# Optimization experiments

Measured on AMD Instinct MI355X. Metric: run time of the kernel, lower is better.

## Reference

```python
import jax, jax.numpy as jnp
import numpy as np

B, L, P, TPP, D, G = 4, 2, 100, 64, 768, 10  # batch, layers, passages, tokens/passage, hidden, n_tables
T = P * TPP


def setup_inputs() -> dict:
    key = jax.random.key(0)
    ks = jax.random.split(key, 12)
    s = 0.02  # weight init scale
    return {
        "answer_states": jax.random.normal(ks[0], (B, L, 1, D), jnp.float32),
        "query_passage_states": jax.random.normal(ks[1], (B, L, T, D), jnp.float32),
        "passage_masks": (jax.random.uniform(ks[2], (B, P, TPP)) < 0.9).astype(jnp.float32),
        "table_ids": jax.random.randint(ks[3], (B, P), 0, G, dtype=jnp.int32),
        "fusion_scores": jax.random.normal(ks[4], (B, P), jnp.float32),
        # learned params: passage_fnt (3D->D), table_fnt (3D->D), feat_l1 (2D->D), feat_l2 (D->1)
        "W_p": jax.random.normal(ks[5], (3 * D, D), jnp.float32) * s,
        "b_p": jnp.zeros((D,), jnp.float32),
        "W_t": jax.random.normal(ks[6], (3 * D, D), jnp.float32) * s,
        "b_t": jnp.zeros((D,), jnp.float32),
        "W1": jax.random.normal(ks[7], (2 * D, D), jnp.float32) * s,
        "b1": jnp.zeros((D,), jnp.float32),
        "W2": jax.random.normal(ks[8], (D, 1), jnp.float32) * s,
        "b2": jnp.zeros((1,), jnp.float32),
    }


def reference(answer_states, query_passage_states, passage_masks, table_ids,
              fusion_scores, W_p, b_p, W_t, b_t, W1, b1, W2, b2):
    # Use only the last layer, as in forward (states[:, -1:, :, :]).
    a = answer_states[:, -1:, :, :]                 # [B,1,1,D]
    q = query_passage_states[:, -1:, :, :]          # [B,1,T,D]
    a = jnp.broadcast_to(a, q.shape)
    x = jnp.concatenate([a, q, a * q], axis=-1)     # [B,1,T,3D]

    ps = (x @ W_p + b_p).reshape(B, 1, P, TPP, D)   # passage states
    ts = (x @ W_t + b_t).reshape(B, 1, P, TPP, D)   # per-passage table states

    # Group-by table_id max-pool over the passage axis, then broadcast back.
    def aggr_one(ts_i, tid):                        # ts_i: [1,P,TPP,D], tid: [P]
        data = jnp.moveaxis(ts_i, 1, 0)             # [P,1,TPP,D]
        seg_max = jax.ops.segment_max(data, tid, num_segments=G)  # [G,1,TPP,D]
        return jnp.moveaxis(seg_max[tid], 0, 1)     # [1,P,TPP,D]

    aggr = jax.vmap(aggr_one)(ts, table_ids)        # [B,1,P,TPP,D]

    feat = jnp.concatenate([ps, aggr], axis=-1)     # [B,1,P,TPP,2D]
    # feature_fnt: Linear -> ReLU -> (dropout = identity in eval) -> Linear
    h = jax.nn.relu(feat @ W1 + b1)                 # [B,1,P,TPP,D]
    scores = (h @ W2 + b2)[..., 0]                  # [B,1,P,TPP]

    masked = scores * passage_masks[:, None, :, :]  # broadcast mask over layers
    # sum over layers and tokens -> per-passage adapt scores
    out = masked.sum(axis=(1, 3))                   # [B,P]
    return out
```

## Files before the change

kernel.cpp:

```cpp
#include <hip/hip_runtime.h>
#include <hip/hip_bf16.h>

#define B_ 4
#define L_ 2
#define P_ 100
#define TPP_ 64
#define D_ 768
#define G_ 10
#define T_ (P_ * TPP_)
#define NC_ (2 * D_)

typedef __attribute__((ext_vector_type(8))) short bf16x8;
typedef __attribute__((ext_vector_type(4))) float f32x4;

__device__ __forceinline__ unsigned short f2bf(float f) {
    __hip_bfloat16 h = __float2bfloat16(f);
    return *reinterpret_cast<unsigned short*>(&h);
}
__device__ __forceinline__ float bfu2f(unsigned short u) {
    return __uint_as_float(((unsigned int)u) << 16);
}

__device__ __forceinline__ void gload_lds16(const void* g, void* l) {
    __builtin_amdgcn_global_load_lds(
        (const __attribute__((address_space(1))) void*)g,
        (__attribute__((address_space(3))) void*)l, 16, 0, 0);
}

#define SBAR()   __builtin_amdgcn_s_barrier()
#define SCHEDB() __builtin_amdgcn_sched_barrier(0)
#define VMCNT4() asm volatile("s_waitcnt vmcnt(4)" ::: "memory")
#define VMCNT0() asm volatile("s_waitcnt vmcnt(0)" ::: "memory")

__device__ __forceinline__ unsigned int fenc(float v) {
    unsigned int bits = __float_as_uint(v);
    return bits ^ (unsigned int)(((int)bits >> 31) | 0x80000000);
}
__device__ __forceinline__ float fdec(unsigned int k) {
    unsigned int bits = (k & 0x80000000u) ? (k ^ 0x80000000u) : ~k;
    return __uint_as_float(bits);
}

__device__ __forceinline__ void stage64(
    const __hip_bfloat16* __restrict__ Ag, const __hip_bfloat16* __restrict__ Bg,
    int k0, __hip_bfloat16 (*As)[64], __hip_bfloat16 (*Bs)[64],
    int w, int row_l, int soff)
{
#pragma unroll
    for (int j = 0; j < 2; ++j) {
        int r = w * 16 + j * 8 + row_l;
        gload_lds16(Ag + (size_t)r * D_ + k0 + soff, &As[w * 16 + j * 8][0]);
        gload_lds16(Bg + (size_t)r * D_ + k0 + soff, &Bs[w * 16 + j * 8][0]);
    }
}

__device__ __forceinline__ void mfma_step64(
    __hip_bfloat16 (*As)[64], __hip_bfloat16 (*Bs)[64],
    int rr, int h, int wm, int wn, f32x4 acc[4][2])
{
#pragma unroll
    for (int ks = 0; ks < 2; ++ks) {
        const int rsl = (((ks << 2) + h) ^ (rr & 7)) << 3;
        bf16x8 af[4], bfr[2];
#pragma unroll
        for (int mi = 0; mi < 4; ++mi)
            af[mi] = *reinterpret_cast<const bf16x8*>(
                &As[wm * 64 + mi * 16 + rr][rsl]);
#pragma unroll
        for (int ni = 0; ni < 2; ++ni)
            bfr[ni] = *reinterpret_cast<const bf16x8*>(
                &Bs[wn * 32 + ni * 16 + rr][rsl]);
#pragma unroll
        for (int mi = 0; mi < 4; ++mi)
#pragma unroll
            for (int ni = 0; ni < 2; ++ni)
                acc[mi][ni] = __builtin_amdgcn_mfma_f32_16x16x32_bf16(
                    af[mi], bfr[ni], acc[mi][ni], 0, 0, 0);
    }
}

#define MFMA_STEP_P(As, Bs)                                                   \
    __builtin_amdgcn_s_setprio(1);                                            \
    mfma_step64(As, Bs, rr, h, wm, wn, acc);                                  \
    __builtin_amdgcn_s_setprio(0);

#define MFMA_LOOP_PIPE(Ag, Bg)                                                \
    {                                                                         \
        const int rr = lane & 15, h = lane >> 4;                              \
        const int row_l = lane >> 3;                                          \
        const int soff = ((lane & 7) ^ row_l) << 3;                           \
        stage64((Ag), (Bg), 0, As0, Bs0, w, row_l, soff);                     \
        stage64((Ag), (Bg), 64, As1, Bs1, w, row_l, soff);                    \
        SCHEDB();                                                             \
        for (int t = 0; t < 10; t += 2) {                                     \
            VMCNT4(); SBAR(); SCHEDB();                                       \
            MFMA_STEP_P(As0, Bs0);                                            \
            SCHEDB(); SBAR(); SCHEDB();                                       \
            stage64((Ag), (Bg), (t + 2) * 64, As0, Bs0, w, row_l, soff);      \
            SCHEDB();                                                         \
            VMCNT4(); SBAR(); SCHEDB();                                       \
            MFMA_STEP_P(As1, Bs1);                                            \
            SCHEDB(); SBAR(); SCHEDB();                                       \
            stage64((Ag), (Bg), (t + 3) * 64, As1, Bs1, w, row_l, soff);      \
            SCHEDB();                                                         \
        }                                                                     \
        VMCNT4(); SBAR(); SCHEDB();                                           \
        MFMA_STEP_P(As0, Bs0);                                   \
        SCHEDB();                                                             \
        VMCNT0(); SBAR(); SCHEDB();                                           \
        MFMA_STEP_P(As1, Bs1);                                   \
        __syncthreads();                                                      \
    }

#define DECL_LDS_DB()                                                         \
    __shared__ __align__(16) __hip_bfloat16 As0[128][64];                     \
    __shared__ __align__(16) __hip_bfloat16 Bs0[128][64];                     \
    __shared__ __align__(16) __hip_bfloat16 As1[128][64];                     \
    __shared__ __align__(16) __hip_bfloat16 Bs1[128][64];

#define DECL_ACC()                                                            \
    f32x4 acc[4][2];                                                          \
    _Pragma("unroll") for (int i = 0; i < 4; ++i)                             \
        _Pragma("unroll") for (int j = 0; j < 2; ++j)                         \
            _Pragma("unroll") for (int e = 0; e < 4; ++e) acc[i][j][e] = 0.0f;

__global__ __launch_bounds__(256) void prep_all(
    const float* __restrict__ answer, const float* __restrict__ W_p,
    const float* __restrict__ b_p, const float* __restrict__ W_t,
    const float* __restrict__ b_t, const float* __restrict__ W1,
    const float* __restrict__ qps, const float* __restrict__ mask,
    const float* __restrict__ b2,
    __hip_bfloat16* __restrict__ Wpe_nat, __hip_bfloat16* __restrict__ Wbig,
    float* __restrict__ c_p, float* __restrict__ c_t,
    __hip_bfloat16* __restrict__ qb, __hip_bfloat16* __restrict__ W1at,
    __hip_bfloat16* __restrict__ W1bt, unsigned int* __restrict__ smU,
    float* __restrict__ out)
{
    __shared__ float lds[64][65];
    __shared__ float a_s[64];
    __shared__ float red2[2][4][64];

    const int bid = blockIdx.x;
    const int tid = threadIdx.x;

    if (bid < 1152) {
        const int n0 = (bid % 24) * 64;
        const int k0 = ((bid / 24) % 12) * 64;
        const int b  = bid / 288;
        if (tid < 64) a_s[tid] = answer[((size_t)b * L_ + (L_ - 1)) * D_ + k0 + tid];
        __syncthreads();
        if (n0 < D_) {
#pragma unroll
            for (int i = 0; i < 16; ++i) {
                int k = (tid >> 6) + i * 4;
                int n = tid & 63;
                float v = W_p[(size_t)(D_ + k0 + k) * D_ + n0 + n] +
                          a_s[k] * W_p[(size_t)(2 * D_ + k0 + k) * D_ + n0 + n];
                Wpe_nat[(size_t)b * D_ * D_ + (size_t)(k0 + k) * D_ + n0 + n] =
                    __float2bfloat16(v);
            }
        } else {
            const int nn0 = n0 - D_;
#pragma unroll
            for (int i = 0; i < 16; ++i) {
                int k = (tid >> 6) + i * 4;
                int n = tid & 63;
                lds[k][n] = W_t[(size_t)(D_ + k0 + k) * D_ + nn0 + n] +
                            a_s[k] * W_t[(size_t)(2 * D_ + k0 + k) * D_ + nn0 + n];
            }
            __syncthreads();
#pragma unroll
            for (int j = 0; j < 16; ++j) {
                int n = (tid >> 6) + j * 4;
                int kk = tid & 63;
                Wbig[((size_t)b * NC_ + n0 + n) * D_ + k0 + kk] =
                    __float2bfloat16(lds[kk][n]);
            }
        }
    } else if (bid < 1200) {
        const int local = bid - 1152;
        const int b = local / 12;
        const int d = (local % 12) * 64 + (tid & 63);
        const int ks = tid >> 6;
        const float* a = answer + ((size_t)b * L_ + (L_ - 1)) * D_;
        float sp = 0.f, st = 0.f;
#pragma unroll 4
        for (int k = ks; k < D_; k += 4) {
            float av = a[k];
            sp += av * W_p[(size_t)k * D_ + d];
            st += av * W_t[(size_t)k * D_ + d];
        }
        red2[0][ks][tid & 63] = sp;
        red2[1][ks][tid & 63] = st;
        __syncthreads();
        if (ks == 0) {
            float s1 = b_p[d], s2 = b_t[d];
#pragma unroll
            for (int i = 0; i < 4; ++i) {
                s1 += red2[0][i][tid & 63];
                s2 += red2[1][i][tid & 63];
            }
            c_p[b * D_ + d] = s1;
            c_t[b * D_ + d] = s2;
        }
    } else if (bid < 1488) {
        const int local = bid - 1200;
        const int n0 = (local % 12) * 64;
        const int k0 = (local / 12) * 64;
#pragma unroll
        for (int i = 0; i < 16; ++i) {
            int k = (tid >> 6) + i * 4;
            int n = tid & 63;
            lds[k][n] = W1[(size_t)(k0 + k) * D_ + n0 + n];
        }
        __syncthreads();
        __hip_bfloat16* dst = (k0 < D_) ? W1at : W1bt;
        const int kk0 = (k0 < D_) ? k0 : k0 - D_;
#pragma unroll
        for (int j = 0; j < 16; ++j) {
            int n = (tid >> 6) + j * 4;
            int kk = tid & 63;
            dst[(size_t)(n0 + n) * D_ + kk0 + kk] = __float2bfloat16(lds[kk][n]);
        }
    } else if (bid < 1490) {
        int bp = (bid - 1488) * 256 + tid;
        if (bp < B_ * P_) {
            float s = 0.f;
#pragma unroll 8
            for (int t = 0; t < TPP_; ++t) s += mask[(size_t)bp * TPP_ + t];
            out[bp] = s * b2[0];
        }
    } else if (bid < 11090) {
        size_t base = ((size_t)(bid - 1490) * 256 + tid) * 8;
        int b = (int)(base / ((size_t)T_ * D_));
        size_t off = base % ((size_t)T_ * D_);
        const float4* src = reinterpret_cast<const float4*>(
            qps + ((size_t)b * L_ + (L_ - 1)) * (size_t)T_ * D_ + off);
        float4 v0 = src[0], v1 = src[1];
        bf16x8 o;
        o[0] = (short)f2bf(v0.x); o[1] = (short)f2bf(v0.y);
        o[2] = (short)f2bf(v0.z); o[3] = (short)f2bf(v0.w);
        o[4] = (short)f2bf(v1.x); o[5] = (short)f2bf(v1.y);
        o[6] = (short)f2bf(v1.z); o[7] = (short)f2bf(v1.w);
        *reinterpret_cast<bf16x8*>(&qb[base]) = o;
    } else {
        size_t base = ((size_t)(bid - 11090) * 256 + tid) * 8;
        uint4 z = {0u, 0u, 0u, 0u};
        *reinterpret_cast<uint4*>(&smU[base]) = z;
        *reinterpret_cast<uint4*>(&smU[base + 4]) = z;
    }
}

__global__ __launch_bounds__(512) void fused_ts_c1(
    const __hip_bfloat16* __restrict__ qb, __hip_bfloat16* __restrict__ Wbig,
    const float* __restrict__ c_t, const int* __restrict__ tids,
    unsigned int* __restrict__ smU,
    const __hip_bfloat16* __restrict__ W1at,
    const __hip_bfloat16* __restrict__ Wpe_nat,
    const float* __restrict__ c_p, const float* __restrict__ W1,
    const float* __restrict__ b1, float* __restrict__ cc)
{
    DECL_LDS_DB();
    __shared__ float red[8][64];
    const int bid = blockIdx.x;
    const int tid = threadIdx.x;
    const int lane = tid & 63, w = tid >> 6;
    const int wm = w & 1, wn = w >> 1;

    if (bid < 1200) {
        const int swz = (bid & 7) * 150 + (bid >> 3);
        const int tn = swz % 6;
        const int tmb = swz / 6;
        const int tm = tmb % 50, b = tmb / 50;
        DECL_ACC();
        const __hip_bfloat16* Ag = qb + (size_t)b * T_ * D_ + (size_t)tm * 128 * D_;
        const __hip_bfloat16* Bg =
            Wbig + (size_t)b * NC_ * D_ + (size_t)(D_ + tn * 128) * D_;
        MFMA_LOOP_PIPE(Ag, Bg);

        const int p = tm * 2 + wm;
        const int g = tids[b * P_ + p];
        unsigned int* smb = smU + ((size_t)(b * G_ + g) * TPP_) * D_;
        const int h = lane >> 4;
#pragma unroll
        for (int ni = 0; ni < 2; ++ni) {
            int col = tn * 128 + wn * 32 + ni * 16 + (lane & 15);
            float cv = c_t[b * D_ + col];
#pragma unroll
            for (int mi = 0; mi < 4; ++mi)
#pragma unroll
                for (int e = 0; e < 4; ++e) {
                    int t = mi * 16 + h * 4 + e;
                    atomicMax(&smb[(size_t)t * D_ + col],
                              fenc(acc[mi][ni][e] + cv));
                }
        }
    } else if (bid < 1344) {
        const int local = bid - 1200;
        const int tm = local % 6, tn = (local / 6) % 6, b = local / 36;
        DECL_ACC();
        const __hip_bfloat16* Ag = W1at + (size_t)tm * 128 * D_;
        const __hip_bfloat16* Bg =
            Wpe_nat + (size_t)b * D_ * D_ + (size_t)tn * 128 * D_;
        MFMA_LOOP_PIPE(Ag, Bg);
#pragma unroll
        for (int mi = 0; mi < 4; ++mi)
#pragma unroll
            for (int ni = 0; ni < 2; ++ni) {
                int col = tn * 128 + wn * 32 + ni * 16 + (lane & 15);
                int row = tm * 128 + wm * 64 + mi * 16 + (lane >> 4) * 4;
#pragma unroll
                for (int e = 0; e < 4; ++e)
                    Wbig[(size_t)b * NC_ * D_ + (size_t)(row + e) * D_ + col] =
                        __float2bfloat16(acc[mi][ni][e]);
            }
    } else {
        const int local = bid - 1344;
        const int b = local / 12;
        const int n = (local % 12) * 64 + (tid & 63);
        const int ks = tid >> 6;
        float s = 0.f;
#pragma unroll 4
        for (int d = ks; d < D_; d += 8)
            s += c_p[b * D_ + d] * W1[(size_t)d * D_ + n];
        red[ks][tid & 63] = s;
        __syncthreads();
        if (ks == 0) {
            float tot = b1[n];
#pragma unroll
            for (int i = 0; i < 8; ++i) tot += red[i][tid & 63];
            cc[b * D_ + n] = tot;
        }
    }
}

__global__ __launch_bounds__(256) void sm_convert(
    const unsigned int* __restrict__ smU, __hip_bfloat16* __restrict__ sm)
{
    size_t base = ((size_t)blockIdx.x * 256 + threadIdx.x) * 8;
    uint4 u0 = *reinterpret_cast<const uint4*>(&smU[base]);
    uint4 u1 = *reinterpret_cast<const uint4*>(&smU[base + 4]);
    bf16x8 o;
    o[0] = (short)f2bf(fdec(u0.x)); o[1] = (short)f2bf(fdec(u0.y));
    o[2] = (short)f2bf(fdec(u0.z)); o[3] = (short)f2bf(fdec(u0.w));
    o[4] = (short)f2bf(fdec(u1.x)); o[5] = (short)f2bf(fdec(u1.y));
    o[6] = (short)f2bf(fdec(u1.z)); o[7] = (short)f2bf(fdec(u1.w));
    *reinterpret_cast<bf16x8*>(&sm[base]) = o;
}

__global__ __launch_bounds__(512) void gemm_smw(
    const __hip_bfloat16* __restrict__ sm, const __hip_bfloat16* __restrict__ W1bt,
    __hip_bfloat16* __restrict__ smW)
{
    const int swz = (blockIdx.x & 7) * 15 + (blockIdx.x >> 3);
    const int tn = swz % 6, tm = swz / 6;
    DECL_LDS_DB();
    const int tid = threadIdx.x;
    const int lane = tid & 63, w = tid >> 6;
    const int wm = w & 1, wn = w >> 1;
    DECL_ACC();

    const __hip_bfloat16* Ag = sm + (size_t)tm * 128 * D_;
    const __hip_bfloat16* Bg = W1bt + (size_t)tn * 128 * D_;
    MFMA_LOOP_PIPE(Ag, Bg);

#pragma unroll
    for (int mi = 0; mi < 4; ++mi)
#pragma unroll
        for (int ni = 0; ni < 2; ++ni) {
            int col = tn * 128 + wn * 32 + ni * 16 + (lane & 15);
            int rb  = tm * 128 + wm * 64 + mi * 16 + (lane >> 4) * 4;
#pragma unroll
            for (int e = 0; e < 4; ++e)
                smW[(size_t)(rb + e) * D_ + col] = __float2bfloat16(acc[mi][ni][e]);
        }
}

__global__ __launch_bounds__(512) void gemm_fin(
    const __hip_bfloat16* __restrict__ qb, const __hip_bfloat16* __restrict__ Wbig,
    const float* __restrict__ cc, const __hip_bfloat16* __restrict__ smW,
    const int* __restrict__ tids, const float* __restrict__ W2,
    const float* __restrict__ mask, float* __restrict__ out)
{
    const int swz = (blockIdx.x & 7) * 150 + (blockIdx.x >> 3);
    const int tn = swz % 6;
    const int tmb = swz / 6;
    const int tm = tmb % 50, b = tmb / 50;
    DECL_LDS_DB();
    __shared__ float rowsum[4][128];

    const int tid = threadIdx.x;
    const int lane = tid & 63, w = tid >> 6;
    const int wm = w & 1, wn = w >> 1;
    DECL_ACC();

    const __hip_bfloat16* Ag = qb + (size_t)b * T_ * D_ + (size_t)tm * 128 * D_;
    const __hip_bfloat16* Bg = Wbig + (size_t)b * NC_ * D_ + (size_t)tn * 128 * D_;
    MFMA_LOOP_PIPE(Ag, Bg);

    const int p = tm * 2 + wm;
    const int g = tids[b * P_ + p];
    const __hip_bfloat16* smWg = smW + ((size_t)(b * G_ + g) * TPP_) * D_;
    const int h = lane >> 4;

    float rs[4][4];
#pragma unroll
    for (int mi = 0; mi < 4; ++mi)
#pragma unroll
        for (int e = 0; e < 4; ++e) rs[mi][e] = 0.f;

#pragma unroll
    for (int ni = 0; ni < 2; ++ni) {
        int col = tn * 128 + wn * 32 + ni * 16 + (lane & 15);
        float ccv = cc[b * D_ + col];
        float w2v = W2[col];
#pragma unroll
        for (int mi = 0; mi < 4; ++mi)
#pragma unroll
            for (int e = 0; e < 4; ++e) {
                int trow = mi * 16 + h * 4 + e;
                float v = acc[mi][ni][e] + ccv +
                          bfu2f(*reinterpret_cast<const unsigned short*>(
                              &smWg[(size_t)trow * D_ + col]));
                rs[mi][e] += fmaxf(v, 0.f) * w2v;
            }
    }
#pragma unroll
    for (int off = 8; off >= 1; off >>= 1)
#pragma unroll
        for (int mi = 0; mi < 4; ++mi)
#pragma unroll
            for (int e = 0; e < 4; ++e) rs[mi][e] += __shfl_xor(rs[mi][e], off);

    if ((lane & 15) == 0) {
        float* dst = &rowsum[wn][wm * 64];
#pragma unroll
        for (int mi = 0; mi < 4; ++mi)
#pragma unroll
            for (int e = 0; e < 4; ++e)
                dst[mi * 16 + h * 4 + e] = rs[mi][e];
    }
    __syncthreads();

    if (tid < 128) {
        int pp = tid >> 6, t = tid & 63;
        float v = (rowsum[0][tid] + rowsum[1][tid] + rowsum[2][tid] +
                   rowsum[3][tid]) *
                  mask[((size_t)b * P_ + tm * 2 + pp) * TPP_ + t];
#pragma unroll
        for (int off = 32; off >= 1; off >>= 1) v += __shfl_xor(v, off);
        if (t == 0) atomicAdd(&out[b * P_ + tm * 2 + pp], v);
    }
}

extern "C" void kernel_launch(void* const* d_in, const int* in_sizes, int n_in,
                              void* d_out, int out_size, void* d_ws, size_t ws_size,
                              hipStream_t stream)
{
    const float* answer = (const float*)d_in[0];
    const float* qps    = (const float*)d_in[1];
    const float* mask   = (const float*)d_in[2];
    const int*   tids   = (const int*)d_in[3];
    const float* W_p = (const float*)d_in[5];
    const float* b_p = (const float*)d_in[6];
    const float* W_t = (const float*)d_in[7];
    const float* b_t = (const float*)d_in[8];
    const float* W1  = (const float*)d_in[9];
    const float* b1  = (const float*)d_in[10];
    const float* W2  = (const float*)d_in[11];
    const float* b2  = (const float*)d_in[12];
    float* out = (float*)d_out;

    char* ws = (char*)d_ws;
    __hip_bfloat16* Wpe_nat = (__hip_bfloat16*)ws; ws += (size_t)B_ * D_ * D_ * 2;
    __hip_bfloat16* Wbig    = (__hip_bfloat16*)ws; ws += (size_t)B_ * NC_ * D_ * 2;
    float* c_p = (float*)ws;                   ws += (size_t)B_ * D_ * 4;
    float* c_t = (float*)ws;                   ws += (size_t)B_ * D_ * 4;
    float* cc  = (float*)ws;                   ws += (size_t)B_ * D_ * 4;
    __hip_bfloat16* qb = (__hip_bfloat16*)ws;  ws += (size_t)B_ * T_ * D_ * 2;
    unsigned int* smU = (unsigned int*)ws;     ws += (size_t)B_ * G_ * TPP_ * D_ * 4;
    __hip_bfloat16* sm = (__hip_bfloat16*)ws;  ws += (size_t)B_ * G_ * TPP_ * D_ * 2;
    __hip_bfloat16* smW = (__hip_bfloat16*)ws; ws += (size_t)B_ * G_ * TPP_ * D_ * 2;
    __hip_bfloat16* W1at = (__hip_bfloat16*)ws; ws += (size_t)D_ * D_ * 2;
    __hip_bfloat16* W1bt = (__hip_bfloat16*)ws; ws += (size_t)D_ * D_ * 2;

    prep_all<<<12050, 256, 0, stream>>>(
        answer, W_p, b_p, W_t, b_t, W1, qps, mask, b2,
        Wpe_nat, Wbig, c_p, c_t, qb, W1at, W1bt, smU, out);
    fused_ts_c1<<<1392, 512, 0, stream>>>(
        qb, Wbig, c_t, tids, smU, W1at, Wpe_nat, c_p, W1, b1, cc);
    sm_convert<<<960, 256, 0, stream>>>(smU, sm);
    gemm_smw<<<120, 512, 0, stream>>>(sm, W1bt, smW);
    gemm_fin<<<1200, 512, 0, stream>>>(
        qb, Wbig, cc, smW, tids, W2, mask, out);
}
```

Baseline: 165.6 us.

## Restructure gemm_fin to 4 waves with 64x64 warp tiles and K=32 staging

Rewrites the final GEMM kernel to use 256 threads (4 waves) per 128x128 tile, each wave computing a 64x64 sub-tile (4x4 MFMA accumulators) instead of 8 waves at 64x32. LDS staging drops to K=32 slices with a new swizzle and a 24-step double-buffered pipeline. The aim is more MFMA work per LDS fragment load and smaller LDS per block, which could allow more blocks per CU, at the cost of more accumulator registers per thread and shallower K steps with more barriers.

```diff
diff --git a/kernel.cpp b/kernel.cpp
--- a/kernel.cpp
+++ b/kernel.cpp
@@ -124,6 +124,88 @@
         _Pragma("unroll") for (int j = 0; j < 2; ++j)                         \
             _Pragma("unroll") for (int e = 0; e < 4; ++e) acc[i][j][e] = 0.0f;
 
+__device__ __forceinline__ void stage32(
+    const __hip_bfloat16* __restrict__ Ag, const __hip_bfloat16* __restrict__ Bg,
+    int k0, __hip_bfloat16 (*As)[32], __hip_bfloat16 (*Bs)[32],
+    int w, int row16, int soff)
+{
+#pragma unroll
+    for (int j = 0; j < 2; ++j) {
+        int r = w * 32 + j * 16 + row16;
+        gload_lds16(Ag + (size_t)r * D_ + k0 + soff, &As[w * 32 + j * 16][0]);
+        gload_lds16(Bg + (size_t)r * D_ + k0 + soff, &Bs[w * 32 + j * 16][0]);
+    }
+}
+
+__device__ __forceinline__ void mfma_step32(
+    __hip_bfloat16 (*As)[32], __hip_bfloat16 (*Bs)[32],
+    int rr, int rsl, int wm, int wn, f32x4 acc[4][4])
+{
+    bf16x8 af[4], bfr[4];
+#pragma unroll
+    for (int mi = 0; mi < 4; ++mi)
+        af[mi] = *reinterpret_cast<const bf16x8*>(
+            &As[wm * 64 + mi * 16 + rr][rsl]);
+#pragma unroll
+    for (int ni = 0; ni < 4; ++ni)
+        bfr[ni] = *reinterpret_cast<const bf16x8*>(
+            &Bs[wn * 64 + ni * 16 + rr][rsl]);
+#pragma unroll
+    for (int mi = 0; mi < 4; ++mi)
+#pragma unroll
+        for (int ni = 0; ni < 4; ++ni)
+            acc[mi][ni] = __builtin_amdgcn_mfma_f32_16x16x32_bf16(
+                af[mi], bfr[ni], acc[mi][ni], 0, 0, 0);
+}
+
+#define MFMA_STEP32_P(As, Bs)                                                 \
+    __builtin_amdgcn_s_setprio(1);                                            \
+    mfma_step32(As, Bs, rr, rsl, wm, wn, acc);                                \
+    __builtin_amdgcn_s_setprio(0);
+
+#define MFMA_LOOP_PIPE32(Ag, Bg)                                              \
+    {                                                                         \
+        const int rr = lane & 15, h = lane >> 4;                              \
+        const int row16 = lane >> 2;                                          \
+        const int soff = ((lane & 3) ^ ((lane >> 3) & 3)) << 3;               \
+        const int rsl = (h ^ ((rr >> 1) & 3)) << 3;                           \
+        stage32((Ag), (Bg), 0,  Cs0, Ds0, w, row16, soff);                    \
+        stage32((Ag), (Bg), 32, Cs1, Ds1, w, row16, soff);                    \
+        SCHEDB();                                                             \
+        for (int t = 0; t < 22; t += 2) {                                     \
+            VMCNT4(); SBAR(); SCHEDB();                                       \
+            MFMA_STEP32_P(Cs0, Ds0);                                          \
+            SCHEDB(); SBAR(); SCHEDB();                                       \
+            stage32((Ag), (Bg), (t + 2) * 32, Cs0, Ds0, w, row16, soff);      \
+            SCHEDB();                                                         \
+            VMCNT4(); SBAR(); SCHEDB();                                       \
+            MFMA_STEP32_P(Cs1, Ds1);                                          \
+            SCHEDB(); SBAR(); SCHEDB();                                       \
+            if (t + 3 < 24)                                                   \
+                stage32((Ag), (Bg), (t + 3) * 32, Cs1, Ds1, w, row16, soff);  \
+            SCHEDB();                                                         \
+        }                                                                     \
+        VMCNT4(); SBAR(); SCHEDB();                                           \
+        MFMA_STEP32_P(Cs0, Ds0);                                 \
+        SCHEDB();                                                             \
+        VMCNT0(); SBAR(); SCHEDB();                                           \
+        MFMA_STEP32_P(Cs1, Ds1);                                 \
+        __syncthreads();                                                      \
+    }
+
+
+#define DECL_LDS_DB32()                                                       \
+    __shared__ __align__(16) __hip_bfloat16 Cs0[128][32];                     \
+    __shared__ __align__(16) __hip_bfloat16 Ds0[128][32];                     \
+    __shared__ __align__(16) __hip_bfloat16 Cs1[128][32];                     \
+    __shared__ __align__(16) __hip_bfloat16 Ds1[128][32];
+
+#define DECL_ACC44()                                                          \
+    f32x4 acc[4][4];                                                          \
+    _Pragma("unroll") for (int i = 0; i < 4; ++i)                             \
+        _Pragma("unroll") for (int j = 0; j < 4; ++j)                         \
+            _Pragma("unroll") for (int e = 0; e < 4; ++e) acc[i][j][e] = 0.0f;
+
 __global__ __launch_bounds__(256) void prep_all(
     const float* __restrict__ answer, const float* __restrict__ W_p,
     const float* __restrict__ b_p, const float* __restrict__ W_t,
@@ -376,7 +458,7 @@
         }
 }
 
-__global__ __launch_bounds__(512) void gemm_fin(
+__global__ __launch_bounds__(256) void gemm_fin(
     const __hip_bfloat16* __restrict__ qb, const __hip_bfloat16* __restrict__ Wbig,
     const float* __restrict__ cc, const __hip_bfloat16* __restrict__ smW,
     const int* __restrict__ tids, const float* __restrict__ W2,
@@ -386,17 +468,17 @@
     const int tn = swz % 6;
     const int tmb = swz / 6;
     const int tm = tmb % 50, b = tmb / 50;
-    DECL_LDS_DB();
-    __shared__ float rowsum[4][128];
+    DECL_LDS_DB32();
+    __shared__ float rowsum[2][128];
 
     const int tid = threadIdx.x;
     const int lane = tid & 63, w = tid >> 6;
     const int wm = w & 1, wn = w >> 1;
-    DECL_ACC();
+    DECL_ACC44();
 
     const __hip_bfloat16* Ag = qb + (size_t)b * T_ * D_ + (size_t)tm * 128 * D_;
     const __hip_bfloat16* Bg = Wbig + (size_t)b * NC_ * D_ + (size_t)tn * 128 * D_;
-    MFMA_LOOP_PIPE(Ag, Bg);
+    MFMA_LOOP_PIPE32(Ag, Bg);
 
     const int p = tm * 2 + wm;
     const int g = tids[b * P_ + p];
@@ -410,8 +492,8 @@
         for (int e = 0; e < 4; ++e) rs[mi][e] = 0.f;
 
 #pragma unroll
-    for (int ni = 0; ni < 2; ++ni) {
-        int col = tn * 128 + wn * 32 + ni * 16 + (lane & 15);
+    for (int ni = 0; ni < 4; ++ni) {
+        int col = tn * 128 + wn * 64 + ni * 16 + (lane & 15);
         float ccv = cc[b * D_ + col];
         float w2v = W2[col];
 #pragma unroll
@@ -433,19 +515,17 @@
             for (int e = 0; e < 4; ++e) rs[mi][e] += __shfl_xor(rs[mi][e], off);
 
     if ((lane & 15) == 0) {
-        float* dst = &rowsum[wn][wm * 64];
 #pragma unroll
         for (int mi = 0; mi < 4; ++mi)
 #pragma unroll
             for (int e = 0; e < 4; ++e)
-                dst[mi * 16 + h * 4 + e] = rs[mi][e];
+                rowsum[wn][wm * 64 + mi * 16 + h * 4 + e] = rs[mi][e];
     }
     __syncthreads();
 
     if (tid < 128) {
         int pp = tid >> 6, t = tid & 63;
-        float v = (rowsum[0][tid] + rowsum[1][tid] + rowsum[2][tid] +
-                   rowsum[3][tid]) *
+        float v = (rowsum[0][tid] + rowsum[1][tid]) *
                   mask[((size_t)b * P_ + tm * 2 + pp) * TPP_ + t];
 #pragma unroll
         for (int off = 32; off >= 1; off >>= 1) v += __shfl_xor(v, off);
@@ -491,6 +571,6 @@
         qb, Wbig, c_t, tids, smU, W1at, Wpe_nat, c_p, W1, b1, cc);
     sm_convert<<<960, 256, 0, stream>>>(smU, sm);
     gemm_smw<<<120, 512, 0, stream>>>(sm, W1bt, smW);
-    gemm_fin<<<1200, 512, 0, stream>>>(
+    gemm_fin<<<1200, 256, 0, stream>>>(
         qb, Wbig, cc, smW, tids, W2, mask, out);
 }
```

Measured after the change: 171.2 us. +3.4%, slower.
